# Optimization experiments

Measured on AMD Instinct MI355X. Metric: run time of the kernel, lower is better.

Reference implementation:

```python
import jax, jax.numpy as jnp
import numpy as np

N_POINTS = 8192
N_DIM = 2
N_PAIRS = 262144


def setup_inputs() -> dict:
    key = jax.random.key(0)
    k1, k2, k3, k4 = jax.random.split(key, 4)
    logits = jax.random.normal(k1, (N_POINTS, N_DIM), dtype=jnp.float32)
    i = jax.random.randint(k2, (N_PAIRS,), 0, N_POINTS, dtype=jnp.int64)
    j = jax.random.randint(k3, (N_PAIRS,), 0, N_POINTS, dtype=jnp.int64)
    pij = jax.random.uniform(k4, (N_PAIRS,), dtype=jnp.float32, minval=1e-6, maxval=1.0)
    pij = pij / jnp.sum(pij)  # joint probabilities, strictly positive
    return {"pij": pij, "i": i, "j": j, "logits": logits}


def reference(pij, i, j, logits):
    # Pairwise squared distances via the norm expansion (same math as the
    # N x N x D expanded-subtract in the torch original, without the huge tensor).
    sq = jnp.sum(logits * logits, axis=1)                      # [N]
    dkl2 = sq[:, None] + sq[None, :] - 2.0 * (logits @ logits.T)  # [N, N]
    n_diag = logits.shape[0]
    # Student-t partition function, excluding the diagonal (each diag term is 1).
    part = jnp.sum(1.0 / (1.0 + dkl2)) - n_diag
    xi = logits[i]                                              # [E, D]
    xj = logits[j]                                              # [E, D]
    # NOTE: torch adds 1.0 elementwise BEFORE summing over D, so this is
    # (D + ||xi-xj||^2)^-1 — reproduced faithfully.
    num = 1.0 / jnp.sum(1.0 + (xi - xj) ** 2, axis=1)           # [E]
    qij = num / part
    return jnp.sum(pij * (jnp.log(pij) - jnp.log(qij)))
```

## Files before the change

kernel.cpp:

```cpp
#include <hip/hip_runtime.h>
#include <math.h>

#define N_POINTS 8192
#define N_PAIRS  262144

constexpr int BLOCKS  = 512;
constexpr int THREADS = 256;
constexpr int RPB     = N_POINTS / BLOCKS;
constexpr int RPT     = 4;
constexpr int GROUPS  = RPB / RPT;
constexpr int TPG     = THREADS / GROUPS;
constexpr int EPB     = N_PAIRS / BLOCKS;

__global__ __launch_bounds__(THREADS)
void fused_kernel(const float* __restrict__ logits,
                  const float* __restrict__ pij,
                  const int* __restrict__ ei,
                  const int* __restrict__ ej,
                  float* __restrict__ partials) {
    __shared__ float2 pts[N_POINTS];
    __shared__ float wred[3][THREADS / 64];

    const int t = threadIdx.x;
    const int b = blockIdx.x;

    {
        const float4* src = (const float4*)logits;
        float4* dst = (float4*)pts;
        #pragma unroll
        for (int k = t; k < N_POINTS / 2; k += THREADS) dst[k] = src[k];
    }
    __syncthreads();

    const int g  = t / TPG;
    const int c  = t % TPG;
    const int r0 = b * RPB + g * RPT;

    const float2 p0 = pts[r0 + 0];
    const float2 p1 = pts[r0 + 1];
    const float2 p2 = pts[r0 + 2];
    const float2 p3 = pts[r0 + 3];

    float a0 = 0.f, a1 = 0.f, a2 = 0.f, a3 = 0.f;
    #pragma unroll 4
    for (int k = c; k < N_POINTS; k += TPG) {
        const float2 q = pts[k];
        float dx, dy, d2;
        dx = p0.x - q.x; dy = p0.y - q.y;
        d2 = __builtin_fmaf(dx, dx, __builtin_fmaf(dy, dy, 1.0f));
        a0 += __builtin_amdgcn_rcpf(d2);
        dx = p1.x - q.x; dy = p1.y - q.y;
        d2 = __builtin_fmaf(dx, dx, __builtin_fmaf(dy, dy, 1.0f));
        a1 += __builtin_amdgcn_rcpf(d2);
        dx = p2.x - q.x; dy = p2.y - q.y;
        d2 = __builtin_fmaf(dx, dx, __builtin_fmaf(dy, dy, 1.0f));
        a2 += __builtin_amdgcn_rcpf(d2);
        dx = p3.x - q.x; dy = p3.y - q.y;
        d2 = __builtin_fmaf(dx, dx, __builtin_fmaf(dy, dy, 1.0f));
        a3 += __builtin_amdgcn_rcpf(d2);
    }
    float part = (a0 + a1) + (a2 + a3);

    float s1 = 0.0f, sp = 0.0f;
    #pragma unroll
    for (int it = 0; it < EPB / THREADS; ++it) {
        const int e = b * EPB + it * THREADS + t;
        const int ia = ei[e];
        const int ib = ej[e];
        const float2 pa = pts[ia];
        const float2 pb = pts[ib];
        const float dx = pa.x - pb.x;
        const float dy = pa.y - pb.y;
        const float d2 = __builtin_fmaf(dx, dx, __builtin_fmaf(dy, dy, 2.0f));
        const float p  = pij[e];
        s1 += p * (__logf(p) + __logf(d2));
        sp += p;
    }

    #pragma unroll
    for (int off = 32; off > 0; off >>= 1) {
        part += __shfl_down(part, off, 64);
        s1   += __shfl_down(s1,   off, 64);
        sp   += __shfl_down(sp,   off, 64);
    }
    const int w = t >> 6, l = t & 63;
    if (l == 0) { wred[0][w] = part; wred[1][w] = s1; wred[2][w] = sp; }
    __syncthreads();
    if (t == 0) {
        float r0s = 0.f, r1s = 0.f, r2s = 0.f;
        #pragma unroll
        for (int i = 0; i < THREADS / 64; ++i) {
            r0s += wred[0][i]; r1s += wred[1][i]; r2s += wred[2][i];
        }
        partials[0 * BLOCKS + b] = r0s;
        partials[1 * BLOCKS + b] = r1s;
        partials[2 * BLOCKS + b] = r2s;
    }
}

__global__ __launch_bounds__(256)
void final_kernel(const float* __restrict__ partials, float* __restrict__ out) {
    __shared__ double ra[4], rs[4], rp[4];
    const int t = threadIdx.x;

    double a = (double)partials[0 * BLOCKS + t] + (double)partials[0 * BLOCKS + t + 256];
    double s = (double)partials[1 * BLOCKS + t] + (double)partials[1 * BLOCKS + t + 256];
    double p = (double)partials[2 * BLOCKS + t] + (double)partials[2 * BLOCKS + t + 256];

    #pragma unroll
    for (int off = 32; off > 0; off >>= 1) {
        a += __shfl_down(a, off, 64);
        s += __shfl_down(s, off, 64);
        p += __shfl_down(p, off, 64);
    }
    const int w = t >> 6, l = t & 63;
    if (l == 0) { ra[w] = a; rs[w] = s; rp[w] = p; }
    __syncthreads();
    if (t == 0) {
        double A = 0.0, S = 0.0, P = 0.0;
        #pragma unroll
        for (int i = 0; i < 4; ++i) { A += ra[i]; S += rs[i]; P += rp[i]; }
        A -= (double)N_POINTS;
        out[0] = (float)(S + log(A) * P);
    }
}

extern "C" void kernel_launch(void* const* d_in, const int* in_sizes, int n_in,
                              void* d_out, int out_size, void* d_ws, size_t ws_size,
                              hipStream_t stream) {
    const float* pij    = (const float*)d_in[0];
    const int*   ei     = (const int*)d_in[1];
    const int*   ej     = (const int*)d_in[2];
    const float* logits = (const float*)d_in[3];
    float* out = (float*)d_out;

    float* partials = (float*)d_ws;

    fused_kernel<<<BLOCKS, THREADS, 0, stream>>>(logits, pij, ei, ej, partials);
    final_kernel<<<1, 256, 0, stream>>>(partials, out);
}
```

Baseline: 78.23 us.

## Exploit symmetry of pairwise kernel to halve partition-function work

Rewrites the N×N partition sum to use the symmetry of the Student-t kernel. Each block sweeps two 8-row tiles, paired so the triangular workloads balance, over only the columns at or after the tile start. The sum is doubled and the diagonal tile blocks are subtracted once. This roughly halves the reciprocal and FMA work. The edge loop also switches to vectorized int2/float2 loads of two pairs per thread.

```diff
diff --git a/kernel.cpp b/kernel.cpp
--- a/kernel.cpp
+++ b/kernel.cpp
@@ -6,10 +6,8 @@
 
 constexpr int BLOCKS  = 512;
 constexpr int THREADS = 256;
-constexpr int RPB     = N_POINTS / BLOCKS;
-constexpr int RPT     = 4;
-constexpr int GROUPS  = RPB / RPT;
-constexpr int TPG     = THREADS / GROUPS;
+constexpr int TILE    = 8;
+constexpr int NTILES  = N_POINTS / TILE;
 constexpr int EPB     = N_PAIRS / BLOCKS;
 
 __global__ __launch_bounds__(THREADS)
@@ -32,49 +30,66 @@
     }
     __syncthreads();
 
-    const int g  = t / TPG;
-    const int c  = t % TPG;
-    const int r0 = b * RPB + g * RPT;
+    const int v1 = b;
+    const int v2 = NTILES - 1 - b;
 
-    const float2 p0 = pts[r0 + 0];
-    const float2 p1 = pts[r0 + 1];
-    const float2 p2 = pts[r0 + 2];
-    const float2 p3 = pts[r0 + 3];
+    auto sweep = [&](int v) -> float {
+        const int r0 = v * TILE;
+        float rx[TILE], ry[TILE];
+        #pragma unroll
+        for (int r = 0; r < TILE; ++r) { rx[r] = pts[r0 + r].x; ry[r] = pts[r0 + r].y; }
+        float a[TILE];
+        #pragma unroll
+        for (int r = 0; r < TILE; ++r) a[r] = 0.0f;
+        #pragma unroll 2
+        for (int k = r0 + t; k < N_POINTS; k += THREADS) {
+            const float2 q = pts[k];
+            #pragma unroll
+            for (int r = 0; r < TILE; ++r) {
+                const float dx = rx[r] - q.x;
+                const float dy = ry[r] - q.y;
+                const float d2 = __builtin_fmaf(dx, dx, __builtin_fmaf(dy, dy, 1.0f));
+                a[r] += __builtin_amdgcn_rcpf(d2);
+            }
+        }
+        float s = 0.0f;
+        #pragma unroll
+        for (int r = 0; r < TILE; ++r) s += a[r];
+        return s;
+    };
 
-    float a0 = 0.f, a1 = 0.f, a2 = 0.f, a3 = 0.f;
-    #pragma unroll 4
-    for (int k = c; k < N_POINTS; k += TPG) {
-        const float2 q = pts[k];
-        float dx, dy, d2;
-        dx = p0.x - q.x; dy = p0.y - q.y;
-        d2 = __builtin_fmaf(dx, dx, __builtin_fmaf(dy, dy, 1.0f));
-        a0 += __builtin_amdgcn_rcpf(d2);
-        dx = p1.x - q.x; dy = p1.y - q.y;
-        d2 = __builtin_fmaf(dx, dx, __builtin_fmaf(dy, dy, 1.0f));
-        a1 += __builtin_amdgcn_rcpf(d2);
-        dx = p2.x - q.x; dy = p2.y - q.y;
-        d2 = __builtin_fmaf(dx, dx, __builtin_fmaf(dy, dy, 1.0f));
-        a2 += __builtin_amdgcn_rcpf(d2);
-        dx = p3.x - q.x; dy = p3.y - q.y;
-        d2 = __builtin_fmaf(dx, dx, __builtin_fmaf(dy, dy, 1.0f));
-        a3 += __builtin_amdgcn_rcpf(d2);
+    float T = sweep(v1) + sweep(v2);
+
+    float Dc = 0.0f;
+    if (t < 128) {
+        const int v = (t < 64) ? v1 : v2;
+        const int l = t & 63;
+        const int i = v * TILE + (l >> 3);
+        const int k = v * TILE + (l & 7);
+        const float dx = pts[i].x - pts[k].x;
+        const float dy = pts[i].y - pts[k].y;
+        const float d2 = __builtin_fmaf(dx, dx, __builtin_fmaf(dy, dy, 1.0f));
+        Dc = __builtin_amdgcn_rcpf(d2);
     }
-    float part = (a0 + a1) + (a2 + a3);
+    float part = __builtin_fmaf(2.0f, T, -Dc);
 
     float s1 = 0.0f, sp = 0.0f;
-    #pragma unroll
-    for (int it = 0; it < EPB / THREADS; ++it) {
-        const int e = b * EPB + it * THREADS + t;
-        const int ia = ei[e];
-        const int ib = ej[e];
-        const float2 pa = pts[ia];
-        const float2 pb = pts[ib];
-        const float dx = pa.x - pb.x;
-        const float dy = pa.y - pb.y;
-        const float d2 = __builtin_fmaf(dx, dx, __builtin_fmaf(dy, dy, 2.0f));
-        const float p  = pij[e];
-        s1 += p * (__logf(p) + __logf(d2));
-        sp += p;
+    {
+        const int2   ea = ((const int2*)(ei + b * EPB))[t];
+        const int2   eb = ((const int2*)(ej + b * EPB))[t];
+        const float2 pp = ((const float2*)(pij + b * EPB))[t];
+
+        float2 pa = pts[ea.x], pb = pts[eb.x];
+        float dx = pa.x - pb.x, dy = pa.y - pb.y;
+        float d2 = __builtin_fmaf(dx, dx, __builtin_fmaf(dy, dy, 2.0f));
+        s1 += pp.x * (__logf(pp.x) + __logf(d2));
+        sp += pp.x;
+
+        pa = pts[ea.y]; pb = pts[eb.y];
+        dx = pa.x - pb.x; dy = pa.y - pb.y;
+        d2 = __builtin_fmaf(dx, dx, __builtin_fmaf(dy, dy, 2.0f));
+        s1 += pp.y * (__logf(pp.y) + __logf(d2));
+        sp += pp.y;
     }
 
     #pragma unroll
```

New measurement: 73.03 us. 1.07x faster.
